# Kernel tuning notes

Hardware: AMD Instinct MI355X
Metric: run time of the kernel (lower is better)

## Reference

```python
import jax, jax.numpy as jnp
import numpy as np

N = 50000      # nodes
E = 800000     # edges
D_IN = 128
D_H = 128
D_OUT = 64


def _glorot(key, fan_in, fan_out):
    s = float(np.sqrt(6.0 / (fan_in + fan_out)))
    return jax.random.uniform(key, (fan_in, fan_out), jnp.float32, -s, s)


def setup_inputs() -> dict:
    key = jax.random.key(0)
    ks = jax.random.split(key, 8)
    x = jax.random.normal(ks[0], (N, D_IN), jnp.float32)
    edge_index = jax.random.randint(ks[1], (2, E), 0, N, dtype=jnp.int32)
    return {
        "x": x,
        "edge_index": edge_index,
        "W0": _glorot(ks[2], D_IN, D_H), "b0": jnp.zeros((D_H,), jnp.float32),
        "W1": _glorot(ks[3], D_H, D_H),  "b1": jnp.zeros((D_H,), jnp.float32),
        "W2": _glorot(ks[4], D_H, D_H),  "b2": jnp.zeros((D_H,), jnp.float32),
        "W_out": _glorot(ks[5], D_H, D_OUT), "b_out": jnp.zeros((D_OUT,), jnp.float32),
    }


def reference(x, edge_index, W0, b0, W1, b1, W2, b2, W_out, b_out):
    src = edge_index[0]
    dst = edge_index[1]
    # GCN normalization with self-loops: deg = in-degree(dst) + 1
    deg = jax.ops.segment_sum(jnp.ones((E,), x.dtype), dst, num_segments=N) + 1.0
    dinv = jax.lax.rsqrt(deg)                       # [N]
    edge_coef = (dinv[src] * dinv[dst])[:, None]    # [E,1]
    self_coef = (dinv * dinv)[:, None]              # [N,1]

    def gcn_conv(h, W, b):
        h = h @ W                                            # [N,F]
        agg = jax.ops.segment_sum(h[src] * edge_coef, dst, num_segments=N)
        agg = agg + h * self_coef                            # self-loop term
        return agg + b

    h = x
    for W, b in ((W0, b0), (W1, b1), (W2, b2)):
        h_in = h
        h = jax.nn.relu(gcn_conv(h, W, b))  # eval mode: dropout is identity
        if h.shape == h_in.shape:
            h = h + h_in
    return h @ W_out + b_out
```

## Files before the change

kernel.cpp:

```cpp
#include <hip/hip_runtime.h>

#define N_NODES 50000
#define N_EDGES 800000
#define NB512 98

static inline int cdiv(int a, int b) { return (a + b - 1) / b; }

typedef __attribute__((ext_vector_type(8))) short s8vec;
typedef __attribute__((ext_vector_type(4))) float f32x4;

__device__ inline ushort f2b(float f) {
    uint u = __float_as_uint(f);
    uint r = (u + 0x7fffu + ((u >> 16) & 1u)) >> 16;
    return (ushort)r;
}
__device__ inline float b2f_lo(uint v) { return __uint_as_float(v << 16); }
__device__ inline float b2f_hi(uint v) { return __uint_as_float(v & 0xffff0000u); }

__device__ inline void add8(float* acc, uint4 v) {
    acc[0] += b2f_lo(v.x); acc[1] += b2f_hi(v.x);
    acc[2] += b2f_lo(v.y); acc[3] += b2f_hi(v.y);
    acc[4] += b2f_lo(v.z); acc[5] += b2f_hi(v.z);
    acc[6] += b2f_lo(v.w); acc[7] += b2f_hi(v.w);
}


__global__ __launch_bounds__(256) void k_prep(int* cnt,
                                              const float* __restrict__ W0, const float* __restrict__ W1,
                                              const float* __restrict__ W2, const float* __restrict__ Wo,
                                              ushort* Wt0, ushort* Wt1, ushort* Wt2, ushort* Wto) {
    int b = blockIdx.x;
    if (b < 196) {
        int i = b * 256 + threadIdx.x;
        if (i < N_NODES) cnt[i] = 0;
        return;
    }
    int i = (b - 196) * 256 + threadIdx.x;
    if (i < 16384) {
        int nn = i >> 7, k = i & 127;
        Wt0[i] = f2b(W0[k * 128 + nn]);
    } else if (i < 32768) {
        int j = i - 16384; int nn = j >> 7, k = j & 127;
        Wt1[j] = f2b(W1[k * 128 + nn]);
    } else if (i < 49152) {
        int j = i - 32768; int nn = j >> 7, k = j & 127;
        Wt2[j] = f2b(W2[k * 128 + nn]);
    } else if (i < 57344) {
        int j = i - 49152; int nn = j >> 7, k = j & 127;
        Wto[j] = f2b(Wo[k * 64 + nn]);
    }
}

__global__ __launch_bounds__(256) void k_count(const int* __restrict__ dst, int* cnt,
                                               int* __restrict__ rank, int e) {
    int i = blockIdx.x * 256 + threadIdx.x;
    if (i < e) rank[i] = atomicAdd(&cnt[dst[i]], 1);
}


__global__ __launch_bounds__(512) void k_scan_all(const int* __restrict__ cnt,
                                                  int* rowptr, float* dinv,
                                                  int n, int e, int nb) {
    __shared__ int sh[512];
    int t = threadIdx.x, b = blockIdx.x;
    int start = b * 512;

    int partial = 0;
    for (int i = t; i < start; i += 512) partial += cnt[i];
    sh[t] = partial;
    __syncthreads();
    for (int off = 256; off > 0; off >>= 1) {
        if (t < off) sh[t] += sh[t + off];
        __syncthreads();
    }
    int base = sh[0];
    __syncthreads();

    int i = start + t;
    int v = (i < n) ? cnt[i] : 0;
    sh[t] = v;
    __syncthreads();
    for (int off = 1; off < 512; off <<= 1) {
        int add = (t >= off) ? sh[t - off] : 0;
        __syncthreads();
        sh[t] += add;
        __syncthreads();
    }
    if (i < n) {
        rowptr[i] = base + sh[t] - v;
        dinv[i] = rsqrtf((float)v + 1.0f);
    }
    if (b == nb - 1 && t == 0) rowptr[n] = e;
}


template <int NCOL, bool IN_F32, bool OUT_F32, bool SCALE>
__device__ inline void mm_body(const void* __restrict__ Av, const ushort* __restrict__ Wt,
                               const float* __restrict__ bias, const float* __restrict__ dinv,
                               void* __restrict__ Cv, int n, int bid) {
    constexpr int NT = NCOL / 16;
    int wave = threadIdx.x >> 6;
    int lane = threadIdx.x & 63;
    int quad = lane >> 4;
    int lm = lane & 15;
    int row0 = bid * 128 + wave * 32;

    int rA0 = row0 + lm;      if (rA0 > n - 1) rA0 = n - 1;
    int rA1 = row0 + 16 + lm; if (rA1 > n - 1) rA1 = n - 1;

    f32x4 acc[2][NT];
#pragma unroll
    for (int r = 0; r < 2; r++)
#pragma unroll
        for (int t = 0; t < NT; t++) acc[r][t] = (f32x4){0.f, 0.f, 0.f, 0.f};

    for (int kc = 0; kc < 128; kc += 32) {
        s8vec af[2];
        if (IN_F32) {
            const float* A = (const float*)Av;
#pragma unroll
            for (int r = 0; r < 2; r++) {
                const float* p = A + (size_t)(r ? rA1 : rA0) * 128 + quad * 8 + kc;
                float4 a = *(const float4*)p, b = *(const float4*)(p + 4);
                s8vec v;
                v[0] = (short)f2b(a.x); v[1] = (short)f2b(a.y);
                v[2] = (short)f2b(a.z); v[3] = (short)f2b(a.w);
                v[4] = (short)f2b(b.x); v[5] = (short)f2b(b.y);
                v[6] = (short)f2b(b.z); v[7] = (short)f2b(b.w);
                af[r] = v;
            }
        } else {
            const ushort* A = (const ushort*)Av;
            af[0] = *(const s8vec*)(A + (size_t)rA0 * 128 + quad * 8 + kc);
            af[1] = *(const s8vec*)(A + (size_t)rA1 * 128 + quad * 8 + kc);
        }
#pragma unroll
        for (int t = 0; t < NT; t++) {
            s8vec bf = *(const s8vec*)(Wt + (size_t)(t * 16 + lm) * 128 + kc + quad * 8);
            acc[0][t] = __builtin_amdgcn_mfma_f32_16x16x32_bf16(af[0], bf, acc[0][t], 0, 0, 0);
            acc[1][t] = __builtin_amdgcn_mfma_f32_16x16x32_bf16(af[1], bf, acc[1][t], 0, 0, 0);
        }
    }

#pragma unroll
    for (int r = 0; r < 2; r++) {
#pragma unroll
        for (int i = 0; i < 4; i++) {
            int rr = row0 + r * 16 + quad * 4 + i;
            if (rr < n) {
                float dv = SCALE ? dinv[rr] : 1.0f;
#pragma unroll
                for (int t = 0; t < NT; t++) {
                    int col = t * 16 + lm;
                    if (OUT_F32)
                        ((float*)Cv)[(size_t)rr * NCOL + col] = acc[r][t][i] + bias[col];
                    else
                        ((ushort*)Cv)[(size_t)rr * 128 + col] =
                            f2b(SCALE ? acc[r][t][i] * dv : acc[r][t][i]);
                }
            }
        }
    }
}

__global__ __launch_bounds__(256) void k_mm0_fill(const void* __restrict__ Av,
                                                  const ushort* __restrict__ Wt,
                                                  const float* __restrict__ dinv,
                                                  void* __restrict__ Cv, int n, int mmblocks,
                                                  const int* __restrict__ src, const int* __restrict__ dst,
                                                  const int* __restrict__ rank,
                                                  const int* __restrict__ rowptr,
                                                  ushort* ed, int e) {
    if ((int)blockIdx.x >= mmblocks) {
        int base = ((int)blockIdx.x - mmblocks) * 1024 + threadIdx.x;
#pragma unroll
        for (int k = 0; k < 4; k++) {
            int i = base + k * 256;
            if (i < e) {
                int d = dst[i];
                int pos = rowptr[d] + rank[i];
                ed[pos] = (ushort)src[i];
            }
        }
        return;
    }
    mm_body<128, true, false, true>(Av, Wt, nullptr, dinv, Cv, n, blockIdx.x);
}


template <int NCOL, bool RES_F32, bool FINAL>
__global__ __launch_bounds__(256) void k_gather_mm(const uint4* __restrict__ T4,
                                                   const int* __restrict__ rowptr,
                                                   const ushort* __restrict__ ed,
                                                   const float* __restrict__ dinv,
                                                   const float* __restrict__ biasL,
                                                   const void* __restrict__ resv,
                                                   uint4* __restrict__ hout,
                                                   const ushort* __restrict__ Wt,
                                                   const float* __restrict__ bias_out,
                                                   void* __restrict__ Cv, int n) {
    __shared__ uint4 As4[16 * 17];
    ushort* As = (ushort*)As4;

    int tid = threadIdx.x;
    int nl = tid >> 4, ql = tid & 15;
    int qb = tid & 48;
    int node = blockIdx.x * 16 + nl;

    float acc[8] = {0.f, 0.f, 0.f, 0.f, 0.f, 0.f, 0.f, 0.f};
    int beg = rowptr[node], end = rowptr[node + 1];

    for (int base = beg; base < end; base += 16) {
        int m = end - base; if (m > 16) m = 16;
        int idx = base + ql; if (idx > end - 1) idx = end - 1;
        uint em = ed[idx];
        int j = 0;
        for (; j + 4 <= m; j += 4) {
            int s0 = __shfl((int)em, qb + j);
            int s1 = __shfl((int)em, qb + j + 1);
            int s2 = __shfl((int)em, qb + j + 2);
            int s3 = __shfl((int)em, qb + j + 3);
            uint4 v0 = T4[(size_t)s0 * 16 + ql];
            uint4 v1 = T4[(size_t)s1 * 16 + ql];
            uint4 v2 = T4[(size_t)s2 * 16 + ql];
            uint4 v3 = T4[(size_t)s3 * 16 + ql];
            add8(acc, v0); add8(acc, v1); add8(acc, v2); add8(acc, v3);
        }
        for (; j < m; j++) {
            int s = __shfl((int)em, qb + j);
            uint4 v = T4[(size_t)s * 16 + ql];
            add8(acc, v);
        }
    }

    uint4 vs = T4[(size_t)node * 16 + ql];
    add8(acc, vs);

    float di = dinv[node];
    float4 bv0 = ((const float4*)biasL)[ql * 2];
    float4 bv1 = ((const float4*)biasL)[ql * 2 + 1];
    float bb[8] = {bv0.x, bv0.y, bv0.z, bv0.w, bv1.x, bv1.y, bv1.z, bv1.w};

    float r[8];
    if (RES_F32) {
        float4 r0 = ((const float4*)resv)[(size_t)node * 32 + ql * 2];
        float4 r1 = ((const float4*)resv)[(size_t)node * 32 + ql * 2 + 1];
        r[0] = r0.x; r[1] = r0.y; r[2] = r0.z; r[3] = r0.w;
        r[4] = r1.x; r[5] = r1.y; r[6] = r1.z; r[7] = r1.w;
    } else {
        uint4 rv = ((const uint4*)resv)[(size_t)node * 16 + ql];
        r[0] = b2f_lo(rv.x); r[1] = b2f_hi(rv.x); r[2] = b2f_lo(rv.y); r[3] = b2f_hi(rv.y);
        r[4] = b2f_lo(rv.z); r[5] = b2f_hi(rv.z); r[6] = b2f_lo(rv.w); r[7] = b2f_hi(rv.w);
    }

    float o[8];
#pragma unroll
    for (int i = 0; i < 8; i++)
        o[i] = fmaxf(acc[i] * di + bb[i], 0.f) + r[i];

    uint4 ov;
    ov.x = (uint)f2b(o[0]) | ((uint)f2b(o[1]) << 16);
    ov.y = (uint)f2b(o[2]) | ((uint)f2b(o[3]) << 16);
    ov.z = (uint)f2b(o[4]) | ((uint)f2b(o[5]) << 16);
    ov.w = (uint)f2b(o[6]) | ((uint)f2b(o[7]) << 16);

    if (!FINAL) hout[(size_t)node * 16 + ql] = ov;
    *(uint4*)&As[nl * 136 + ql * 8] = ov;
    __syncthreads();

    constexpr int NT = NCOL / 64;
    int wave = tid >> 6;
    int lane = tid & 63;
    int quad = lane >> 4;
    int lm = lane & 15;

    f32x4 macc[NT];
#pragma unroll
    for (int t = 0; t < NT; t++) macc[t] = (f32x4){0.f, 0.f, 0.f, 0.f};

    for (int kc = 0; kc < 128; kc += 32) {
        s8vec af = *(const s8vec*)&As[lm * 136 + kc + quad * 8];
#pragma unroll
        for (int t = 0; t < NT; t++) {
            int col = wave * (16 * NT) + t * 16 + lm;
            s8vec bf = *(const s8vec*)(Wt + (size_t)col * 128 + kc + quad * 8);
            macc[t] = __builtin_amdgcn_mfma_f32_16x16x32_bf16(af, bf, macc[t], 0, 0, 0);
        }
    }

    int row0 = blockIdx.x * 16;
#pragma unroll
    for (int t = 0; t < NT; t++) {
        int col = wave * (16 * NT) + t * 16 + lm;
#pragma unroll
        for (int i = 0; i < 4; i++) {
            int rr = row0 + quad * 4 + i;
            if (FINAL)
                ((float*)Cv)[(size_t)rr * 64 + col] = macc[t][i] + bias_out[col];
            else
                ((ushort*)Cv)[(size_t)rr * 128 + col] = f2b(macc[t][i] * dinv[rr]);
        }
    }
}


extern "C" void kernel_launch(void* const* d_in, const int* in_sizes, int n_in,
                              void* d_out, int out_size, void* d_ws, size_t ws_size,
                              hipStream_t stream) {
    const float* x  = (const float*)d_in[0];
    const int* eidx = (const int*)d_in[1];
    const float* W0 = (const float*)d_in[2];
    const float* b0 = (const float*)d_in[3];
    const float* W1 = (const float*)d_in[4];
    const float* b1 = (const float*)d_in[5];
    const float* W2 = (const float*)d_in[6];
    const float* b2 = (const float*)d_in[7];
    const float* Wo = (const float*)d_in[8];
    const float* bo = (const float*)d_in[9];
    float* out = (float*)d_out;

    const int N = N_NODES, E = N_EDGES;
    const int* srcI = eidx;
    const int* dstI = eidx + E;

    char* ws = (char*)d_ws;
    auto alloc = [&](size_t bytes) { char* p = ws; ws += (bytes + 255) / 256 * 256; return p; };
    int*    cnt    = (int*)alloc((size_t)N * 4);
    int*    rowptr = (int*)alloc((size_t)(N + 1) * 4);
    int*    rank   = (int*)alloc((size_t)E * 4);
    float*  dinv   = (float*)alloc((size_t)N * 4);
    ushort* ed     = (ushort*)alloc((size_t)E * 2);
    ushort* tA     = (ushort*)alloc((size_t)N * 128 * 2);
    ushort* tB     = (ushort*)alloc((size_t)N * 128 * 2);
    ushort* hAb    = (ushort*)alloc((size_t)N * 128 * 2);
    ushort* hBb    = (ushort*)alloc((size_t)N * 128 * 2);
    ushort* Wt0    = (ushort*)alloc(128 * 128 * 2);
    ushort* Wt1    = (ushort*)alloc(128 * 128 * 2);
    ushort* Wt2    = (ushort*)alloc(128 * 128 * 2);
    ushort* Wto    = (ushort*)alloc(64 * 128 * 2);

    dim3 b256(256), b512(512);

    const int mmGrid   = cdiv(N, 128);
    const int fillGrid = cdiv(E, 1024);
    const int gGrid    = N / 16;

    k_prep<<<196 + 224, b256, 0, stream>>>(cnt, W0, W1, W2, Wo, Wt0, Wt1, Wt2, Wto);
    k_count<<<cdiv(E, 256), b256, 0, stream>>>(dstI, cnt, rank, E);
    k_scan_all<<<NB512, b512, 0, stream>>>(cnt, rowptr, dinv, N, E, NB512);

    k_mm0_fill<<<mmGrid + fillGrid, b256, 0, stream>>>(x, Wt0, dinv, tA, N, mmGrid,
                                                       srcI, dstI, rank, rowptr, ed, E);

    k_gather_mm<128, true, false><<<gGrid, b256, 0, stream>>>(
        (const uint4*)tA, rowptr, ed, dinv, b0, x, (uint4*)hAb, Wt1, nullptr, tB, N);

    k_gather_mm<128, false, false><<<gGrid, b256, 0, stream>>>(
        (const uint4*)tB, rowptr, ed, dinv, b1, hAb, (uint4*)hBb, Wt2, nullptr, tA, N);

    k_gather_mm<64, false, true><<<gGrid, b256, 0, stream>>>(
        (const uint4*)tA, rowptr, ed, dinv, b2, hBb, nullptr, Wto, bo, out, N);
}
```

Baseline: 276.2 us.

## Group nodes by in-degree via permutation to balance gather-mm blocks

Builds a degree histogram during the scan, prefix-scans it, and fills a permutation that sorts nodes into degree bins. The three gather+matmul kernels then process nodes through this permutation, so the 16 nodes in a block have similar edge counts and the block's loop lengths match. This targets imbalance inside a block, where one high-degree node stalls the rest. The cost is an extra tiny kernel, atomics, and scattered (non-contiguous) row reads and writes of the residual and output tensors.

```diff
diff --git a/kernel.cpp b/kernel.cpp
--- a/kernel.cpp
+++ b/kernel.cpp
@@ -3,6 +3,7 @@
 #define N_NODES 50000
 #define N_EDGES 800000
 #define NB512 98
+#define DBINS 64
 
 static inline int cdiv(int a, int b) { return (a + b - 1) / b; }
 
@@ -25,7 +26,7 @@
 }
 
 
-__global__ __launch_bounds__(256) void k_prep(int* cnt,
+__global__ __launch_bounds__(256) void k_prep(int* cnt, int* dhist,
                                               const float* __restrict__ W0, const float* __restrict__ W1,
                                               const float* __restrict__ W2, const float* __restrict__ Wo,
                                               ushort* Wt0, ushort* Wt1, ushort* Wt2, ushort* Wto) {
@@ -33,6 +34,7 @@
     if (b < 196) {
         int i = b * 256 + threadIdx.x;
         if (i < N_NODES) cnt[i] = 0;
+        if (b == 0 && threadIdx.x < DBINS) dhist[threadIdx.x] = 0;
         return;
     }
     int i = (b - 196) * 256 + threadIdx.x;
@@ -59,11 +61,13 @@
 
 
 __global__ __launch_bounds__(512) void k_scan_all(const int* __restrict__ cnt,
-                                                  int* rowptr, float* dinv,
+                                                  int* rowptr, float* dinv, int* dhist,
                                                   int n, int e, int nb) {
     __shared__ int sh[512];
+    __shared__ int lh[DBINS];
     int t = threadIdx.x, b = blockIdx.x;
     int start = b * 512;
+    if (t < DBINS) lh[t] = 0;
 
     int partial = 0;
     for (int i = t; i < start; i += 512) partial += cnt[i];
@@ -89,8 +93,26 @@
     if (i < n) {
         rowptr[i] = base + sh[t] - v;
         dinv[i] = rsqrtf((float)v + 1.0f);
-    }
+        atomicAdd(&lh[v < DBINS ? v : DBINS - 1], 1);
+    }
+    __syncthreads();
+    if (t < DBINS && lh[t]) atomicAdd(&dhist[t], lh[t]);
     if (b == nb - 1 && t == 0) rowptr[n] = e;
+}
+
+__global__ __launch_bounds__(64) void k_dscan(const int* __restrict__ dhist, int* dcur) {
+    __shared__ int sh[DBINS];
+    int t = threadIdx.x;
+    int v = dhist[t];
+    sh[t] = v;
+    __syncthreads();
+    for (int off = 1; off < DBINS; off <<= 1) {
+        int add = (t >= off) ? sh[t - off] : 0;
+        __syncthreads();
+        sh[t] += add;
+        __syncthreads();
+    }
+    dcur[t] = sh[t] - v;
 }
 
 
@@ -166,13 +188,25 @@
 __global__ __launch_bounds__(256) void k_mm0_fill(const void* __restrict__ Av,
                                                   const ushort* __restrict__ Wt,
                                                   const float* __restrict__ dinv,
-                                                  void* __restrict__ Cv, int n, int mmblocks,
+                                                  void* __restrict__ Cv, int n, int mmblocks, int fillblocks,
                                                   const int* __restrict__ src, const int* __restrict__ dst,
                                                   const int* __restrict__ rank,
                                                   const int* __restrict__ rowptr,
-                                                  ushort* ed, int e) {
-    if ((int)blockIdx.x >= mmblocks) {
-        int base = ((int)blockIdx.x - mmblocks) * 1024 + threadIdx.x;
+                                                  ushort* ed,
+                                                  const int* __restrict__ cnt, int* dcur, int* perm, int e) {
+    int b = blockIdx.x;
+    if (b >= mmblocks + fillblocks) {
+        int i = (b - mmblocks - fillblocks) * 256 + threadIdx.x;
+        if (i < n) {
+            int deg = cnt[i];
+            int bin = deg < DBINS ? deg : DBINS - 1;
+            int pos = atomicAdd(&dcur[bin], 1);
+            perm[pos] = i;
+        }
+        return;
+    }
+    if (b >= mmblocks) {
+        int base = (b - mmblocks) * 1024 + threadIdx.x;
 #pragma unroll
         for (int k = 0; k < 4; k++) {
             int i = base + k * 256;
@@ -184,7 +218,7 @@
         }
         return;
     }
-    mm_body<128, true, false, true>(Av, Wt, nullptr, dinv, Cv, n, blockIdx.x);
+    mm_body<128, true, false, true>(Av, Wt, nullptr, dinv, Cv, n, b);
 }
 
 
@@ -198,14 +232,17 @@
                                                    uint4* __restrict__ hout,
                                                    const ushort* __restrict__ Wt,
                                                    const float* __restrict__ bias_out,
-                                                   void* __restrict__ Cv, int n) {
+                                                   void* __restrict__ Cv,
+                                                   const int* __restrict__ perm, int n) {
     __shared__ uint4 As4[16 * 17];
+    __shared__ int pnode[16];
     ushort* As = (ushort*)As4;
 
     int tid = threadIdx.x;
     int nl = tid >> 4, ql = tid & 15;
     int qb = tid & 48;
-    int node = blockIdx.x * 16 + nl;
+    int node = perm[blockIdx.x * 16 + nl];
+    if (ql == 0) pnode[nl] = node;
 
     float acc[8] = {0.f, 0.f, 0.f, 0.f, 0.f, 0.f, 0.f, 0.f};
     int beg = rowptr[node], end = rowptr[node + 1];
@@ -288,13 +325,12 @@
         }
     }
 
-    int row0 = blockIdx.x * 16;
 #pragma unroll
     for (int t = 0; t < NT; t++) {
         int col = wave * (16 * NT) + t * 16 + lm;
 #pragma unroll
         for (int i = 0; i < 4; i++) {
-            int rr = row0 + quad * 4 + i;
+            int rr = pnode[quad * 4 + i];
             if (FINAL)
                 ((float*)Cv)[(size_t)rr * 64 + col] = macc[t][i] + bias_out[col];
             else
@@ -328,6 +364,9 @@
     int*    cnt    = (int*)alloc((size_t)N * 4);
     int*    rowptr = (int*)alloc((size_t)(N + 1) * 4);
     int*    rank   = (int*)alloc((size_t)E * 4);
+    int*    dhist  = (int*)alloc(DBINS * 4);
+    int*    dcur   = (int*)alloc(DBINS * 4);
+    int*    perm   = (int*)alloc((size_t)N * 4);
     float*  dinv   = (float*)alloc((size_t)N * 4);
     ushort* ed     = (ushort*)alloc((size_t)E * 2);
     ushort* tA     = (ushort*)alloc((size_t)N * 128 * 2);
@@ -343,21 +382,23 @@
 
     const int mmGrid   = cdiv(N, 128);
     const int fillGrid = cdiv(E, 1024);
+    const int permGrid = cdiv(N, 256);
     const int gGrid    = N / 16;
 
-    k_prep<<<196 + 224, b256, 0, stream>>>(cnt, W0, W1, W2, Wo, Wt0, Wt1, Wt2, Wto);
+    k_prep<<<196 + 224, b256, 0, stream>>>(cnt, dhist, W0, W1, W2, Wo, Wt0, Wt1, Wt2, Wto);
     k_count<<<cdiv(E, 256), b256, 0, stream>>>(dstI, cnt, rank, E);
-    k_scan_all<<<NB512, b512, 0, stream>>>(cnt, rowptr, dinv, N, E, NB512);
-
-    k_mm0_fill<<<mmGrid + fillGrid, b256, 0, stream>>>(x, Wt0, dinv, tA, N, mmGrid,
-                                                       srcI, dstI, rank, rowptr, ed, E);
+    k_scan_all<<<NB512, b512, 0, stream>>>(cnt, rowptr, dinv, dhist, N, E, NB512);
+    k_dscan<<<1, 64, 0, stream>>>(dhist, dcur);
+
+    k_mm0_fill<<<mmGrid + fillGrid + permGrid, b256, 0, stream>>>(
+        x, Wt0, dinv, tA, N, mmGrid, fillGrid, srcI, dstI, rank, rowptr, ed, cnt, dcur, perm, E);
 
     k_gather_mm<128, true, false><<<gGrid, b256, 0, stream>>>(
-        (const uint4*)tA, rowptr, ed, dinv, b0, x, (uint4*)hAb, Wt1, nullptr, tB, N);
+        (const uint4*)tA, rowptr, ed, dinv, b0, x, (uint4*)hAb, Wt1, nullptr, tB, perm, N);
 
     k_gather_mm<128, false, false><<<gGrid, b256, 0, stream>>>(
-        (const uint4*)tB, rowptr, ed, dinv, b1, hAb, (uint4*)hBb, Wt2, nullptr, tA, N);
+        (const uint4*)tB, rowptr, ed, dinv, b1, hAb, (uint4*)hBb, Wt2, nullptr, tA, perm, N);
 
     k_gather_mm<64, false, true><<<gGrid, b256, 0, stream>>>(
-        (const uint4*)tA, rowptr, ed, dinv, b2, hBb, nullptr, Wto, bo, out, N);
-}
+        (const uint4*)tA, rowptr, ed, dinv, b2, hBb, nullptr, Wto, bo, out, perm, N);
+}
```

New measurement: 402.7 us. 45.8% more time.
